# Performance work log

Measured on AMD Instinct MI355X. Metric: run time of the kernel, lower is better.

Reference implementation:

```python
import jax, jax.numpy as jnp
import numpy as np

B, T, D, H = 64, 2048, 128, 256  # batch, time, input features, num_cells


def setup_inputs() -> dict:
    key = jax.random.key(0)
    ks = jax.random.split(key, 8)
    w = lambda k, shape: (jax.random.normal(k, shape, dtype=jnp.float32) * 0.05)
    return {
        "x": jax.random.normal(ks[0], (B, T, D), dtype=jnp.float32),
        "k_fwd": w(ks[1], (D, 4 * H)),
        "r_fwd": w(ks[2], (H, 4 * H)),
        "b_fwd": jnp.zeros((4 * H,), jnp.float32),
        "k_bwd": w(ks[3], (D, 4 * H)),
        "r_bwd": w(ks[4], (H, 4 * H)),
        "b_bwd": jnp.zeros((4 * H,), jnp.float32),
        "att_w": jax.random.uniform(ks[5], (H,), dtype=jnp.float32),
    }


def _lstm(x, kernel, rec, bias):
    """Keras-style LSTM (gate order i,f,c,o), return_sequences=True. x: [B,T,D] -> [B,T,H]."""
    xw = jnp.einsum('btd,dk->btk', x, kernel) + bias  # precompute input contribution [B,T,4H]
    h0 = jnp.zeros((x.shape[0], rec.shape[0]), x.dtype)

    def step(carry, xw_t):
        h, c = carry
        z = xw_t + h @ rec  # [B,4H]
        i, f, g, o = jnp.split(z, 4, axis=-1)
        c = jax.nn.sigmoid(f) * c + jax.nn.sigmoid(i) * jnp.tanh(g)
        h = jax.nn.sigmoid(o) * jnp.tanh(c)
        return (h, c), h

    _, hs = jax.lax.scan(step, (h0, h0), jnp.swapaxes(xw, 0, 1))  # hs: [T,B,H]
    return jnp.swapaxes(hs, 0, 1)


def reference(x, k_fwd, r_fwd, b_fwd, k_bwd, r_bwd, b_bwd, att_w):
    # Bidirectional LSTM, merge_mode='sum'
    h_f = _lstm(x, k_fwd, r_fwd, b_fwd)
    h_b = _lstm(x[:, ::-1], k_bwd, r_bwd, b_bwd)[:, ::-1]
    h = h_f + h_b  # [B,T,H]
    # Additive attention pooling (dropout identity at inference)
    m = jnp.tanh(h)
    a = jax.nn.softmax(jnp.einsum('h,bth->bt', att_w, m), axis=-1)  # [B,T]
    r = jnp.einsum('bth,bt->bh', h, a)  # [B,H]
    return jnp.tanh(r)
```

## Files before the change

kernel.cpp:

```cpp
#include <hip/hip_runtime.h>
#include <cstdint>
#include <cstddef>

#define TT 2048
#define DD 128
#define HH 256
#define G4 1024

typedef _Float16 half4_t __attribute__((ext_vector_type(4)));
typedef _Float16 half8_t __attribute__((ext_vector_type(8)));
typedef float floatx4 __attribute__((ext_vector_type(4)));

union H4U64 { uint64_t u; half4_t h; };
union H8U64x2 { uint64_t u[2]; half8_t h; };

__device__ __forceinline__ float sigm(float x) { return 1.f / (1.f + __expf(-x)); }
__device__ __forceinline__ float tanh_f(float x) { return 1.f - 2.f / (1.f + __expf(2.f * x)); }

__device__ __forceinline__ half8_t cvt8(float4 a, float4 b) {
  half8_t v;
  v[0] = (_Float16)a.x; v[1] = (_Float16)a.y; v[2] = (_Float16)a.z; v[3] = (_Float16)a.w;
  v[4] = (_Float16)b.x; v[5] = (_Float16)b.y; v[6] = (_Float16)b.z; v[7] = (_Float16)b.w;
  return v;
}

__global__ void prep_kernel(const float* __restrict__ rf, const float* __restrict__ rb,
                            const float* __restrict__ kf, const float* __restrict__ kb,
                            _Float16* __restrict__ RT, _Float16* __restrict__ KT) {
  int idx = blockIdx.x * 256 + threadIdx.x;
  if (idx < 2 * G4 * HH) {
    int dir = idx >> 18, k = (idx >> 10) & 255, n = idx & 1023;
    const float* src = dir ? rb : rf;
    RT[((size_t)(dir * G4 + n)) * HH + k] = (_Float16)src[(size_t)k * G4 + n];
  } else {
    int i2 = idx - 2 * G4 * HH;
    int dir = i2 >> 17, k = (i2 >> 10) & 127, n = i2 & 1023;
    const float* src = dir ? kb : kf;
    KT[((size_t)(dir * G4 + n)) * DD + k] = (_Float16)src[(size_t)k * G4 + n];
  }
}


#define SENT 0xFFFFFFFFFFFFFFFFull

__global__ __launch_bounds__(256, 1) void lstm_rec_kernel(
    const float* __restrict__ x,
    const float* __restrict__ bias_f, const float* __restrict__ bias_b,
    const _Float16* __restrict__ RT, const _Float16* __restrict__ KT,
    uint64_t* __restrict__ ring, _Float16* __restrict__ hseq) {
  const int bid = blockIdx.x;
  const int split = bid >> 3;
  const int g = bid & 7;
  const int dir = g >> 2;
  const int bg = g & 3;
  const int tid = threadIdx.x;
  const int w = tid >> 6, lane = tid & 63;
  const int lo16 = lane & 15, q = lane >> 4;

  __shared__ _Float16 tile[2][64][20];

  const float* __restrict__ bias = dir ? bias_b : bias_f;

  half8_t bR[4][8], bK[4][4];
  float bgate[4];
#pragma unroll
  for (int gate = 0; gate < 4; ++gate) {
    const int col = gate * 256 + split * 64 + w * 16 + lo16;
    const _Float16* bp = RT + (size_t)(dir * G4 + col) * HH + q * 8;
#pragma unroll
    for (int kk = 0; kk < 8; ++kk) bR[gate][kk] = *reinterpret_cast<const half8_t*>(bp + kk * 32);
    const _Float16* kp = KT + (size_t)(dir * G4 + col) * DD + q * 8;
#pragma unroll
    for (int kx = 0; kx < 4; ++kx) bK[gate][kx] = *reinterpret_cast<const half8_t*>(kp + kx * 32);
    bgate[gate] = bias[col];
  }

  const float* __restrict__ xrow = x + ((size_t)(bg * 16 + lo16) * TT) * DD;

  const int kgl  = tid >> 5;
  const int tb   = (tid >> 1) & 15;
  const int part = tid & 1;
  const int kg_global = split * 8 + kgl;
  const int hofs = split * 64 + kgl * 8 + part * 4;
  const int myofs = (kg_global * 16 + tb) * 2 + part;

  float c[4] = {0.f, 0.f, 0.f, 0.f};

  int tx = dir ? TT - 1 : 0;
  float4 xr[8];
  {
    const float* xp = xrow + (size_t)tx * DD + q * 8;
#pragma unroll
    for (int kx = 0; kx < 4; ++kx) {
      xr[2 * kx]     = *reinterpret_cast<const float4*>(xp + kx * 32);
      xr[2 * kx + 1] = *reinterpret_cast<const float4*>(xp + kx * 32 + 4);
    }
  }
  half8_t ax[4];
#pragma unroll
  for (int kx = 0; kx < 4; ++kx) ax[kx] = cvt8(xr[2 * kx], xr[2 * kx + 1]);

  for (int s = 0; s < TT; ++s) {
    tx = dir ? (TT - 1 - s) : s;

    uint64_t g0[8], g1[8];
    const uint64_t* gp = ring;
    if (s > 0) {
      gp = ring + ((size_t)((((s - 1) & 3) * 8 + g))) * 1024 + (size_t)((q * 16 + lo16) * 2);
#pragma unroll
      for (int kk = 0; kk < 8; ++kk) {
        g0[kk] = __hip_atomic_load(gp + (size_t)kk * 128,     __ATOMIC_RELAXED, __HIP_MEMORY_SCOPE_AGENT);
        g1[kk] = __hip_atomic_load(gp + (size_t)kk * 128 + 1, __ATOMIC_RELAXED, __HIP_MEMORY_SCOPE_AGENT);
      }
    }

    {
      const int sn = (s + 1 < TT) ? s + 1 : s;
      const int txn = dir ? (TT - 1 - sn) : sn;
      const float* xp = xrow + (size_t)txn * DD + q * 8;
#pragma unroll
      for (int kx = 0; kx < 4; ++kx) {
        xr[2 * kx]     = *reinterpret_cast<const float4*>(xp + kx * 32);
        xr[2 * kx + 1] = *reinterpret_cast<const float4*>(xp + kx * 32 + 4);
      }
    }

    floatx4 acc[4];
#pragma unroll
    for (int gate = 0; gate < 4; ++gate) acc[gate] = floatx4{0.f, 0.f, 0.f, 0.f};

#pragma unroll
    for (int kx = 0; kx < 4; ++kx)
#pragma unroll
      for (int gate = 0; gate < 4; ++gate)
        acc[gate] = __builtin_amdgcn_mfma_f32_16x16x32_f16(ax[kx], bK[gate][kx], acc[gate], 0, 0, 0);

    if (s > 0) {
      while (true) {
        bool ok = true;
#pragma unroll
        for (int kk = 0; kk < 8; ++kk) ok = ok & (g0[kk] != SENT) & (g1[kk] != SENT);
        if (__all(ok)) break;
#pragma unroll
        for (int kk = 0; kk < 8; ++kk) {
          if (g0[kk] == SENT)
            g0[kk] = __hip_atomic_load(gp + (size_t)kk * 128,     __ATOMIC_RELAXED, __HIP_MEMORY_SCOPE_AGENT);
          if (g1[kk] == SENT)
            g1[kk] = __hip_atomic_load(gp + (size_t)kk * 128 + 1, __ATOMIC_RELAXED, __HIP_MEMORY_SCOPE_AGENT);
        }
      }

      __hip_atomic_store(ring + ((size_t)((((s + 2) & 3) * 8 + g))) * 1024 + myofs, SENT,
                         __ATOMIC_RELAXED, __HIP_MEMORY_SCOPE_AGENT);

#pragma unroll
      for (int kk = 0; kk < 8; ++kk) {
        H8U64x2 u;
        u.u[0] = g0[kk];
        u.u[1] = g1[kk];
#pragma unroll
        for (int gate = 0; gate < 4; ++gate)
          acc[gate] = __builtin_amdgcn_mfma_f32_16x16x32_f16(u.h, bR[gate][kk], acc[gate], 0, 0, 0);
      }
    }

#pragma unroll
    for (int kx = 0; kx < 4; ++kx) ax[kx] = cvt8(xr[2 * kx], xr[2 * kx + 1]);

    const int par = s & 1;
    {
      half4_t hv4;
#pragma unroll
      for (int r = 0; r < 4; ++r) {
        const float zi = acc[0][r] + bgate[0];
        const float zf = acc[1][r] + bgate[1];
        const float zg = acc[2][r] + bgate[2];
        const float zo = acc[3][r] + bgate[3];
        c[r] = sigm(zf) * c[r] + sigm(zi) * tanh_f(zg);
        hv4[r] = (_Float16)(sigm(zo) * tanh_f(c[r]));
      }
      *reinterpret_cast<half4_t*>(&tile[par][w * 16 + lo16][q * 4]) = hv4;
    }

    asm volatile("s_waitcnt lgkmcnt(0)\n\ts_barrier" ::: "memory");

    {
      H4U64 val;
#pragma unroll
      for (int j = 0; j < 4; ++j) val.h[j] = tile[par][kgl * 8 + part * 4 + j][tb];
      __hip_atomic_store(ring + ((size_t)((s & 3) * 8 + g)) * 1024 + myofs, val.u,
                         __ATOMIC_RELAXED, __HIP_MEMORY_SCOPE_AGENT);
      *reinterpret_cast<uint64_t*>(hseq + ((size_t)g * TT + tx) * (16 * HH) + (size_t)tb * HH + hofs) = val.u;
    }
  }
}


__global__ __launch_bounds__(256) void attn_kernel(const _Float16* __restrict__ h_ex,
                                                   const float* __restrict__ att_w,
                                                   float* __restrict__ out) {
  const int b = blockIdx.x;
  const int bg = b >> 4, b16 = b & 15;
  const int tid = threadIdx.x;
  const int w = tid >> 6, lane = tid & 63;
  __shared__ float sc[TT];
  __shared__ float red[8];
  const size_t ST = 16 * HH;
  const _Float16* __restrict__ hf = h_ex + (size_t)bg * TT * ST + b16 * HH;
  const _Float16* __restrict__ hb = h_ex + (size_t)(4 + bg) * TT * ST + b16 * HH;

  const int h0 = lane * 4;
  const float aw0 = att_w[h0], aw1 = att_w[h0 + 1], aw2 = att_w[h0 + 2], aw3 = att_w[h0 + 3];

  for (int t = w; t < TT; t += 4) {
    half4_t f4 = *reinterpret_cast<const half4_t*>(hf + (size_t)t * ST + h0);
    half4_t b4 = *reinterpret_cast<const half4_t*>(hb + (size_t)t * ST + h0);
    float s = aw0 * tanh_f((float)f4[0] + (float)b4[0])
            + aw1 * tanh_f((float)f4[1] + (float)b4[1])
            + aw2 * tanh_f((float)f4[2] + (float)b4[2])
            + aw3 * tanh_f((float)f4[3] + (float)b4[3]);
#pragma unroll
    for (int off = 32; off >= 1; off >>= 1) s += __shfl_xor(s, off);
    if (lane == 0) sc[t] = s;
  }
  __syncthreads();

  float m = -1e30f;
  for (int i = tid; i < TT; i += 256) m = fmaxf(m, sc[i]);
#pragma unroll
  for (int off = 32; off >= 1; off >>= 1) m = fmaxf(m, __shfl_xor(m, off));
  if (lane == 0) red[w] = m;
  __syncthreads();
  m = fmaxf(fmaxf(red[0], red[1]), fmaxf(red[2], red[3]));

  float ssum = 0.f;
  for (int i = tid; i < TT; i += 256) {
    float e = __expf(sc[i] - m);
    sc[i] = e;
    ssum += e;
  }
#pragma unroll
  for (int off = 32; off >= 1; off >>= 1) ssum += __shfl_xor(ssum, off);
  if (lane == 0) red[4 + w] = ssum;
  __syncthreads();
  const float inv = 1.f / (red[4] + red[5] + red[6] + red[7]);

  float r = 0.f;
  const _Float16* pf = hf + tid;
  const _Float16* pb = hb + tid;
  for (int t = 0; t < TT; ++t)
    r += sc[t] * ((float)pf[(size_t)t * ST] + (float)pb[(size_t)t * ST]);
  out[b * HH + tid] = tanh_f(r * inv);
}


extern "C" void kernel_launch(void* const* d_in, const int* in_sizes, int n_in,
                              void* d_out, int out_size, void* d_ws, size_t ws_size,
                              hipStream_t stream) {
  const float* x     = (const float*)d_in[0];
  const float* k_fwd = (const float*)d_in[1];
  const float* r_fwd = (const float*)d_in[2];
  const float* b_fwd = (const float*)d_in[3];
  const float* k_bwd = (const float*)d_in[4];
  const float* r_bwd = (const float*)d_in[5];
  const float* b_bwd = (const float*)d_in[6];
  const float* att_w = (const float*)d_in[7];
  float* out = (float*)d_out;

  const size_t RT_bytes   = (size_t)2 * G4 * HH * sizeof(_Float16);
  const size_t KT_bytes   = (size_t)2 * G4 * DD * sizeof(_Float16);
  const size_t ring_bytes = (size_t)4 * 8 * 1024 * sizeof(uint64_t);
  char* ws = (char*)d_ws;
  _Float16* RT    = (_Float16*)ws;
  _Float16* KT    = (_Float16*)(ws + RT_bytes);
  uint64_t* ring  = (uint64_t*)(ws + RT_bytes + KT_bytes);
  _Float16* hseq  = (_Float16*)(ws + RT_bytes + KT_bytes + ring_bytes);

  hipMemsetAsync(ring, 0xFF, ring_bytes, stream);
  hipLaunchKernelGGL(prep_kernel, dim3(3072), dim3(256), 0, stream,
                     r_fwd, r_bwd, k_fwd, k_bwd, RT, KT);
  hipLaunchKernelGGL(lstm_rec_kernel, dim3(32), dim3(256), 0, stream,
                     x, b_fwd, b_bwd, RT, KT, ring, hseq);
  hipLaunchKernelGGL(attn_kernel, dim3(64), dim3(256), 0, stream, hseq, att_w, out);
}
```

Baseline: 7.402 ms.

## Interleave two batch groups per block to hide recurrent sync latency

```diff
diff --git a/kernel.cpp b/kernel.cpp
--- a/kernel.cpp
+++ b/kernel.cpp
@@ -43,21 +43,122 @@
 
 #define SENT 0xFFFFFFFFFFFFFFFFull
 
+#define PHASE(CH, gX, xrowX, g0X, g1X, xrX, cX)                                        \
+  {                                                                                    \
+    const int tx = dir ? (TT - 1 - s) : s;                                             \
+                    \
+    half8_t ax[4];                                                                     \
+    _Pragma("unroll")                                                                  \
+    for (int kx = 0; kx < 4; ++kx) ax[kx] = cvt8(xrX[2 * kx], xrX[2 * kx + 1]);        \
+    floatx4 acc[4];                                                                    \
+    _Pragma("unroll")                                                                  \
+    for (int gate = 0; gate < 4; ++gate) acc[gate] = floatx4{0.f, 0.f, 0.f, 0.f};      \
+                                                                      \
+    _Pragma("unroll")                                                                  \
+    for (int kx = 0; kx < 4; ++kx)                                                     \
+      _Pragma("unroll")                                                                \
+      for (int gate = 0; gate < 4; ++gate)                                             \
+        acc[gate] = __builtin_amdgcn_mfma_f32_16x16x32_f16(ax[kx], bK[gate][kx],       \
+                                                           acc[gate], 0, 0, 0);        \
+    if (s > 0) {                                                                       \
+                  \
+      const uint64_t* gp = ring + ((size_t)((((s - 1) & 3) * 8 + gX))) * 1024          \
+                         + (size_t)((q * 16 + lo16) * 2);                              \
+      while (true) {                                                                   \
+        bool ok = true;                                                                \
+        _Pragma("unroll")                                                              \
+        for (int kk = 0; kk < 8; ++kk) ok = ok & (g0X[kk] != SENT) & (g1X[kk] != SENT);\
+        if (__all(ok)) break;                                                          \
+        _Pragma("unroll")                                                              \
+        for (int kk = 0; kk < 8; ++kk) {                                               \
+          if (g0X[kk] == SENT)                                                         \
+            g0X[kk] = __hip_atomic_load(gp + (size_t)kk * 128,                         \
+                                        __ATOMIC_RELAXED, __HIP_MEMORY_SCOPE_AGENT);   \
+          if (g1X[kk] == SENT)                                                         \
+            g1X[kk] = __hip_atomic_load(gp + (size_t)kk * 128 + 1,                     \
+                                        __ATOMIC_RELAXED, __HIP_MEMORY_SCOPE_AGENT);   \
+        }                                                                              \
+      }                                                                                \
+           \
+      __hip_atomic_store(ring + ((size_t)((((s + 2) & 3) * 8 + gX))) * 1024 + myofs,   \
+                         SENT, __ATOMIC_RELAXED, __HIP_MEMORY_SCOPE_AGENT);            \
+                                                                          \
+      _Pragma("unroll")                                                                \
+      for (int kk = 0; kk < 8; ++kk) {                                                 \
+        H8U64x2 u;                                                                     \
+        u.u[0] = g0X[kk];                                                              \
+        u.u[1] = g1X[kk];                                                              \
+        _Pragma("unroll")                                                              \
+        for (int gate = 0; gate < 4; ++gate)                                           \
+          acc[gate] = __builtin_amdgcn_mfma_f32_16x16x32_f16(u.h, bR[gate][kk],        \
+                                                             acc[gate], 0, 0, 0);      \
+      }                                                                                \
+    }                                                                                  \
+                             \
+    {                                                                                  \
+      const int sn = (s + 1 < TT) ? s + 1 : s;                                         \
+      const int txn = dir ? (TT - 1 - sn) : sn;                                        \
+      const float* xp = xrowX + (size_t)txn * DD + q * 8;                              \
+      _Pragma("unroll")                                                                \
+      for (int kx = 0; kx < 4; ++kx) {                                                 \
+        xrX[2 * kx]     = *reinterpret_cast<const float4*>(xp + kx * 32);              \
+        xrX[2 * kx + 1] = *reinterpret_cast<const float4*>(xp + kx * 32 + 4);          \
+      }                                                                                \
+    }                                                                                  \
+             \
+    const int par = s & 1;                                                             \
+    {                                                                                  \
+      half4_t hv4;                                                                     \
+      _Pragma("unroll")                                                                \
+      for (int r = 0; r < 4; ++r) {                                                    \
+        const float zi = acc[0][r] + bgate[0];                                         \
+        const float zf = acc[1][r] + bgate[1];                                         \
+        const float zg = acc[2][r] + bgate[2];                                         \
+        const float zo = acc[3][r] + bgate[3];                                         \
+        cX[r] = sigm(zf) * cX[r] + sigm(zi) * tanh_f(zg);                              \
+        hv4[r] = (_Float16)(sigm(zo) * tanh_f(cX[r]));                                 \
+      }                                                                                \
+      *reinterpret_cast<half4_t*>(&tile[CH][par][w * 16 + lo16][q * 4]) = hv4;         \
+    }                                                                                  \
+                               \
+    asm volatile("s_waitcnt lgkmcnt(0)\n\ts_barrier" ::: "memory");                    \
+                 \
+    {                                                                                  \
+      H4U64 val;                                                                       \
+      _Pragma("unroll")                                                                \
+      for (int j = 0; j < 4; ++j) val.h[j] = tile[CH][par][kgl * 8 + part * 4 + j][tb];\
+      __hip_atomic_store(ring + ((size_t)((s & 3) * 8 + gX)) * 1024 + myofs, val.u,    \
+                         __ATOMIC_RELAXED, __HIP_MEMORY_SCOPE_AGENT);                  \
+      *reinterpret_cast<uint64_t*>(hseq + ((size_t)gX * TT + tx) * (16 * HH)           \
+                                   + (size_t)tb * HH + hofs) = val.u;                  \
+      const uint64_t* gq = ring + ((size_t)((s & 3) * 8 + gX)) * 1024                  \
+                         + (size_t)((q * 16 + lo16) * 2);                              \
+      _Pragma("unroll")                                                                \
+      for (int kk = 0; kk < 8; ++kk) {                                                 \
+        g0X[kk] = __hip_atomic_load(gq + (size_t)kk * 128,                             \
+                                    __ATOMIC_RELAXED, __HIP_MEMORY_SCOPE_AGENT);       \
+        g1X[kk] = __hip_atomic_load(gq + (size_t)kk * 128 + 1,                         \
+                                    __ATOMIC_RELAXED, __HIP_MEMORY_SCOPE_AGENT);       \
+      }                                                                                \
+    }                                                                                  \
+  }
+
 __global__ __launch_bounds__(256, 1) void lstm_rec_kernel(
     const float* __restrict__ x,
     const float* __restrict__ bias_f, const float* __restrict__ bias_b,
     const _Float16* __restrict__ RT, const _Float16* __restrict__ KT,
     uint64_t* __restrict__ ring, _Float16* __restrict__ hseq) {
   const int bid = blockIdx.x;
-  const int split = bid >> 3;
-  const int g = bid & 7;
-  const int dir = g >> 2;
-  const int bg = g & 3;
+  const int split = bid >> 2;
+  const int dir = (bid >> 1) & 1;
+  const int p = bid & 1;
+  const int bgA = p, bgB = p + 2;
+  const int gA = dir * 4 + bgA, gB = dir * 4 + bgB;
   const int tid = threadIdx.x;
   const int w = tid >> 6, lane = tid & 63;
   const int lo16 = lane & 15, q = lane >> 4;
 
-  __shared__ _Float16 tile[2][64][20];
+  __shared__ _Float16 tile[2][2][64][20];
 
   const float* __restrict__ bias = dir ? bias_b : bias_f;
 
@@ -75,7 +176,8 @@
     bgate[gate] = bias[col];
   }
 
-  const float* __restrict__ xrow = x + ((size_t)(bg * 16 + lo16) * TT) * DD;
+  const float* __restrict__ xrowA = x + ((size_t)(bgA * 16 + lo16) * TT) * DD;
+  const float* __restrict__ xrowB = x + ((size_t)(bgB * 16 + lo16) * TT) * DD;
 
   const int kgl  = tid >> 5;
   const int tb   = (tid >> 1) & 15;
@@ -84,114 +186,27 @@
   const int hofs = split * 64 + kgl * 8 + part * 4;
   const int myofs = (kg_global * 16 + tb) * 2 + part;
 
-  float c[4] = {0.f, 0.f, 0.f, 0.f};
-
-  int tx = dir ? TT - 1 : 0;
-  float4 xr[8];
+  float cA[4] = {0.f, 0.f, 0.f, 0.f};
+  float cB[4] = {0.f, 0.f, 0.f, 0.f};
+  uint64_t g0A[8], g1A[8], g0B[8], g1B[8];
+
+  float4 xrA[8], xrB[8];
   {
-    const float* xp = xrow + (size_t)tx * DD + q * 8;
+    const int tx0 = dir ? TT - 1 : 0;
+    const float* xpA = xrowA + (size_t)tx0 * DD + q * 8;
+    const float* xpB = xrowB + (size_t)tx0 * DD + q * 8;
 #pragma unroll
     for (int kx = 0; kx < 4; ++kx) {
-      xr[2 * kx]     = *reinterpret_cast<const float4*>(xp + kx * 32);
-      xr[2 * kx + 1] = *reinterpret_cast<const float4*>(xp + kx * 32 + 4);
+      xrA[2 * kx]     = *reinterpret_cast<const float4*>(xpA + kx * 32);
+      xrA[2 * kx + 1] = *reinterpret_cast<const float4*>(xpA + kx * 32 + 4);
+      xrB[2 * kx]     = *reinterpret_cast<const float4*>(xpB + kx * 32);
+      xrB[2 * kx + 1] = *reinterpret_cast<const float4*>(xpB + kx * 32 + 4);
     }
   }
-  half8_t ax[4];
-#pragma unroll
-  for (int kx = 0; kx < 4; ++kx) ax[kx] = cvt8(xr[2 * kx], xr[2 * kx + 1]);
 
   for (int s = 0; s < TT; ++s) {
-    tx = dir ? (TT - 1 - s) : s;
-
-    uint64_t g0[8], g1[8];
-    const uint64_t* gp = ring;
-    if (s > 0) {
-      gp = ring + ((size_t)((((s - 1) & 3) * 8 + g))) * 1024 + (size_t)((q * 16 + lo16) * 2);
-#pragma unroll
-      for (int kk = 0; kk < 8; ++kk) {
-        g0[kk] = __hip_atomic_load(gp + (size_t)kk * 128,     __ATOMIC_RELAXED, __HIP_MEMORY_SCOPE_AGENT);
-        g1[kk] = __hip_atomic_load(gp + (size_t)kk * 128 + 1, __ATOMIC_RELAXED, __HIP_MEMORY_SCOPE_AGENT);
-      }
-    }
-
-    {
-      const int sn = (s + 1 < TT) ? s + 1 : s;
-      const int txn = dir ? (TT - 1 - sn) : sn;
-      const float* xp = xrow + (size_t)txn * DD + q * 8;
-#pragma unroll
-      for (int kx = 0; kx < 4; ++kx) {
-        xr[2 * kx]     = *reinterpret_cast<const float4*>(xp + kx * 32);
-        xr[2 * kx + 1] = *reinterpret_cast<const float4*>(xp + kx * 32 + 4);
-      }
-    }
-
-    floatx4 acc[4];
-#pragma unroll
-    for (int gate = 0; gate < 4; ++gate) acc[gate] = floatx4{0.f, 0.f, 0.f, 0.f};
-
-#pragma unroll
-    for (int kx = 0; kx < 4; ++kx)
-#pragma unroll
-      for (int gate = 0; gate < 4; ++gate)
-        acc[gate] = __builtin_amdgcn_mfma_f32_16x16x32_f16(ax[kx], bK[gate][kx], acc[gate], 0, 0, 0);
-
-    if (s > 0) {
-      while (true) {
-        bool ok = true;
-#pragma unroll
-        for (int kk = 0; kk < 8; ++kk) ok = ok & (g0[kk] != SENT) & (g1[kk] != SENT);
-        if (__all(ok)) break;
-#pragma unroll
-        for (int kk = 0; kk < 8; ++kk) {
-          if (g0[kk] == SENT)
-            g0[kk] = __hip_atomic_load(gp + (size_t)kk * 128,     __ATOMIC_RELAXED, __HIP_MEMORY_SCOPE_AGENT);
-          if (g1[kk] == SENT)
-            g1[kk] = __hip_atomic_load(gp + (size_t)kk * 128 + 1, __ATOMIC_RELAXED, __HIP_MEMORY_SCOPE_AGENT);
-        }
-      }
-
-      __hip_atomic_store(ring + ((size_t)((((s + 2) & 3) * 8 + g))) * 1024 + myofs, SENT,
-                         __ATOMIC_RELAXED, __HIP_MEMORY_SCOPE_AGENT);
-
-#pragma unroll
-      for (int kk = 0; kk < 8; ++kk) {
-        H8U64x2 u;
-        u.u[0] = g0[kk];
-        u.u[1] = g1[kk];
-#pragma unroll
-        for (int gate = 0; gate < 4; ++gate)
-          acc[gate] = __builtin_amdgcn_mfma_f32_16x16x32_f16(u.h, bR[gate][kk], acc[gate], 0, 0, 0);
-      }
-    }
-
-#pragma unroll
-    for (int kx = 0; kx < 4; ++kx) ax[kx] = cvt8(xr[2 * kx], xr[2 * kx + 1]);
-
-    const int par = s & 1;
-    {
-      half4_t hv4;
-#pragma unroll
-      for (int r = 0; r < 4; ++r) {
-        const float zi = acc[0][r] + bgate[0];
-        const float zf = acc[1][r] + bgate[1];
-        const float zg = acc[2][r] + bgate[2];
-        const float zo = acc[3][r] + bgate[3];
-        c[r] = sigm(zf) * c[r] + sigm(zi) * tanh_f(zg);
-        hv4[r] = (_Float16)(sigm(zo) * tanh_f(c[r]));
-      }
-      *reinterpret_cast<half4_t*>(&tile[par][w * 16 + lo16][q * 4]) = hv4;
-    }
-
-    asm volatile("s_waitcnt lgkmcnt(0)\n\ts_barrier" ::: "memory");
-
-    {
-      H4U64 val;
-#pragma unroll
-      for (int j = 0; j < 4; ++j) val.h[j] = tile[par][kgl * 8 + part * 4 + j][tb];
-      __hip_atomic_store(ring + ((size_t)((s & 3) * 8 + g)) * 1024 + myofs, val.u,
-                         __ATOMIC_RELAXED, __HIP_MEMORY_SCOPE_AGENT);
-      *reinterpret_cast<uint64_t*>(hseq + ((size_t)g * TT + tx) * (16 * HH) + (size_t)tb * HH + hofs) = val.u;
-    }
+    PHASE(0, gA, xrowA, g0A, g1A, xrA, cA)
+    PHASE(1, gB, xrowB, g0B, g1B, xrB, cB)
   }
 }
 
@@ -279,7 +294,7 @@
   hipMemsetAsync(ring, 0xFF, ring_bytes, stream);
   hipLaunchKernelGGL(prep_kernel, dim3(3072), dim3(256), 0, stream,
                      r_fwd, r_bwd, k_fwd, k_bwd, RT, KT);
-  hipLaunchKernelGGL(lstm_rec_kernel, dim3(32), dim3(256), 0, stream,
+  hipLaunchKernelGGL(lstm_rec_kernel, dim3(16), dim3(256), 0, stream,
                      x, b_fwd, b_bwd, RT, KT, ring, hseq);
   hipLaunchKernelGGL(attn_kernel, dim3(64), dim3(256), 0, stream, hseq, att_w, out);
 }
```

Result: slower. 11.66 ms (+57.6%).
